# Kernel tuning notes

Measured on AMD Instinct MI355X. Metric: run time of the kernel, lower is better.

Reference implementation:

```python
import jax, jax.numpy as jnp
import numpy as np

B, C, H, W = 16, 256, 64, 64
N = 8                      # num_heads
D = C // N                 # key_dim = head_dim = 32
INIT_VAL, HEADS_RANGE = 1.0, 3.0
SCALING = D ** (-0.5)
EPS = 1e-6


def _rel_pos(h, w):
    # RetNetRelPos2d, chunkwise_recurrent=True branch
    ang = 1.0 / 10000 ** jnp.linspace(0.0, 1.0, D // 2)
    ang = jnp.repeat(ang, 2)                                   # [D]
    idx = jnp.arange(h * w, dtype=jnp.float32)
    sin = jnp.sin(idx[:, None] * ang[None, :]).reshape(h, w, D)
    cos = jnp.cos(idx[:, None] * ang[None, :]).reshape(h, w, D)
    decay = jnp.log(1.0 - 2.0 ** (-INIT_VAL - HEADS_RANGE * jnp.arange(N, dtype=jnp.float32) / N))
    def d1(l):
        i = jnp.arange(l, dtype=jnp.float32)
        return jnp.abs(i[:, None] - i[None, :]) * decay[:, None, None]   # [N,l,l]
    return sin, cos, d1(h), d1(w)


def _rotate_every_two(x):
    x1 = x[..., ::2]
    x2 = x[..., 1::2]
    return jnp.stack([-x2, x1], axis=-1).reshape(x.shape)


def _theta_shift(x, sin, cos):
    return x * cos + _rotate_every_two(x) * sin


def _layernorm(x, g, b):
    m = jnp.mean(x, axis=-1, keepdims=True)
    v = jnp.mean((x - m) ** 2, axis=-1, keepdims=True)
    return g * (x - m) * jax.lax.rsqrt(v + EPS) + b


def setup_inputs() -> dict:
    key = jax.random.key(0)
    ks = jax.random.split(key, 8)
    s = 0.02
    def w(k, shape):
        return (jax.random.normal(k, shape, jnp.float32) * s)
    return {
        "x": jax.random.normal(ks[0], (B, C, H, W), jnp.float32),
        "Wq": w(ks[1], (C, C)), "bq": jnp.zeros((C,), jnp.float32),
        "Wk": w(ks[2], (C, C)), "bk": jnp.zeros((C,), jnp.float32),
        "Wv": w(ks[3], (C, C)), "bv": jnp.zeros((C,), jnp.float32),
        "lepe_w": w(ks[4], (5, 5, 1, C)), "lepe_b": jnp.zeros((C,), jnp.float32),
        "Wo": w(ks[5], (C, C)), "bo": jnp.zeros((C,), jnp.float32),
        "Wfc": w(ks[6], (C, C)), "bfc": jnp.zeros((C,), jnp.float32),
        "g1": jnp.ones((C,), jnp.float32), "b1": jnp.zeros((C,), jnp.float32),
        "g2": jnp.ones((C,), jnp.float32), "b2": jnp.zeros((C,), jnp.float32),
    }


def _vrc(x, sin, cos, mask_h, mask_w, Wq, bq, Wk, bk, Wv, bv, lepe_w, lepe_b, Wo, bo):
    # x: [B,H,W,C]
    b, h, w, _ = x.shape
    q = x @ Wq + bq
    k = (x @ Wk + bk) * SCALING
    v = x @ Wv + bv
    # lepe: depthwise 5x5 conv on v (NHWC)
    lepe = jax.lax.conv_general_dilated(
        v, lepe_w, window_strides=(1, 1), padding=((2, 2), (2, 2)),
        dimension_numbers=("NHWC", "HWIO", "NHWC"), feature_group_count=C) + lepe_b
    # [B,N,H,W,D]
    q = q.reshape(b, h, w, N, D).transpose(0, 3, 1, 2, 4)
    k = k.reshape(b, h, w, N, D).transpose(0, 3, 1, 2, 4)
    qr = _theta_shift(q, sin, cos)
    kr = _theta_shift(k, sin, cos)
    # ---- W-axis attention: [B,H,N,W,W] ----
    qr_w = qr.transpose(0, 2, 1, 3, 4)           # [B,H,N,W,D]
    kr_w = kr.transpose(0, 2, 1, 3, 4)
    v5 = v.reshape(b, h, w, N, D).transpose(0, 1, 3, 2, 4)   # [B,H,N,W,D]
    qk_w = jnp.einsum("bhnqd,bhnkd->bhnqk", qr_w, kr_w) + mask_w
    v5 = jnp.einsum("bhnqk,bhnkd->bhnqd", jax.nn.softmax(qk_w, axis=-1), v5)
    # ---- H-axis attention: [B,W,N,H,H] ----
    qr_h = qr.transpose(0, 3, 1, 2, 4)           # [B,W,N,H,D]
    kr_h = kr.transpose(0, 3, 1, 2, 4)
    v6 = v5.transpose(0, 3, 2, 1, 4)             # [B,W,N,H,D]
    qk_h = jnp.einsum("bwnqd,bwnkd->bwnqk", qr_h, kr_h) + mask_h
    out = jnp.einsum("bwnqk,bwnkd->bwnqd", jax.nn.softmax(qk_h, axis=-1), v6)
    out = out.transpose(0, 3, 1, 2, 4).reshape(b, h, w, C)   # [B,H,W,C]
    return (out + lepe) @ Wo + bo


def reference(x, Wq, bq, Wk, bk, Wv, bv, lepe_w, lepe_b, Wo, bo, Wfc, bfc, g1, b1, g2, b2):
    xt = x.transpose(0, 2, 3, 1)                 # [B,H,W,C]
    sin, cos, mask_h, mask_w = _rel_pos(H, W)
    y = _vrc(xt, sin, cos, mask_h, mask_w, Wq, bq, Wk, bk, Wv, bv, lepe_w, lepe_b, Wo, bo)
    xt = _layernorm(xt + y, g1, b1)
    xt = _layernorm(xt + (xt @ Wfc + bfc), g2, b2)
    return xt.transpose(0, 3, 1, 2)              # [B,C,H,W]
```

## Files before the change

kernel.cpp:

```cpp
#include <hip/hip_runtime.h>
#include <math.h>

#define B_ 16
#define C_ 256
#define N_ 8
#define D_ 32
#define M_ (B_*64*64)
#define SCALING 0.17677669529663687f

typedef short  bf16x8 __attribute__((ext_vector_type(8)));
typedef float  f32x4  __attribute__((ext_vector_type(4)));
typedef unsigned short u16x8 __attribute__((ext_vector_type(8)));

__device__ __forceinline__ unsigned short f2bf(float f) {
    unsigned u = __float_as_uint(f);
    u += 0x7fffu + ((u >> 16) & 1u);
    return (unsigned short)(u >> 16);
}
__device__ __forceinline__ float bf2f(unsigned short h) {
    return __uint_as_float(((unsigned)h) << 16);
}
__device__ __forceinline__ void gld16(const void* g, void* l) {
    __builtin_amdgcn_global_load_lds(
        (const __attribute__((address_space(1))) unsigned*)g,
        (__attribute__((address_space(3))) unsigned*)l, 16, 0, 0);
}

__global__ __launch_bounds__(256) void k_tables(float* __restrict__ sint,
                                                float* __restrict__ cost)
{
    int t = blockIdx.x * 256 + threadIdx.x;
    int p = t >> 5, d = t & 31;
    int j = d >> 1;
    float ang = (float)pow(10000.0, -(double)j / 15.0);
    float arg = (float)p * ang;
    sint[t] = sinf(arg);
    cost[t] = cosf(arg);
}

__global__ __launch_bounds__(256) void k_wcvt(
    const float* __restrict__ Wq, const float* __restrict__ Wk,
    const float* __restrict__ Wv, const float* __restrict__ Wo,
    const float* __restrict__ Wfc,
    unsigned short* __restrict__ Wqt, unsigned short* __restrict__ Wkt,
    unsigned short* __restrict__ Wvt, unsigned short* __restrict__ Wot,
    unsigned short* __restrict__ Wfct)
{
    __shared__ float t[32][33];
    int z = blockIdx.z;
    const float* W = z==0?Wq : z==1?Wk : z==2?Wv : z==3?Wo : Wfc;
    unsigned short* Wt = z==0?Wqt : z==1?Wkt : z==2?Wvt : z==3?Wot : Wfct;
    float sc = (z==1) ? SCALING : 1.0f;
    int tx = threadIdx.x & 31, ty = threadIdx.x >> 5;
    int bx = blockIdx.x * 32;
    int by = blockIdx.y * 32;
    #pragma unroll
    for (int j = 0; j < 4; ++j)
        t[ty + j*8][tx] = W[(by + ty + j*8) * 256 + bx + tx];
    __syncthreads();
    #pragma unroll
    for (int j = 0; j < 4; ++j)
        Wt[(bx + ty + j*8) * 256 + by + tx] = f2bf(t[tx][ty + j*8] * sc);
}

__global__ __launch_bounds__(256) void k_prep(const float* __restrict__ x,
                                              float* __restrict__ xt,
                                              unsigned short* __restrict__ xbf)
{
    __shared__ float t[32][33];
    int tx = threadIdx.x & 31, ty = threadIdx.x >> 5;
    int bx = blockIdx.x * 32;
    int by = blockIdx.y * 32;
    size_t bo = (size_t)blockIdx.z * (256*4096);
    #pragma unroll
    for (int j = 0; j < 4; ++j)
        t[ty + j*8][tx] = x[bo + (size_t)(by + ty + j*8) * 4096 + bx + tx];
    __syncthreads();
    #pragma unroll
    for (int j = 0; j < 4; ++j) {
        float v = t[tx][ty + j*8];
        size_t o = bo + (size_t)(bx + ty + j*8) * 256 + by + tx;
        xt[o] = v;
        xbf[o] = f2bf(v);
    }
}

__device__ __forceinline__ void mfma128(
    const unsigned short* A, const unsigned short* Bt, int r0, int c0,
    unsigned short* As, unsigned short* Bs, f32x4 acc[4][4])
{
    const int tid = threadIdx.x;
    const int w = tid >> 6, l = tid & 63;
    const int wr = w >> 1, wc = w & 1;
    const int fr = l & 15, fq = l >> 4;
    const int lrow  = l >> 3;
    const int lunit = (l & 7) ^ lrow;
    const int sw = fr & 7;
    #pragma unroll
    for (int kt = 0; kt < 256; kt += 64) {
        __syncthreads();
        #pragma unroll
        for (int it = 0; it < 4; ++it) {
            int R0 = 32*w + it*8;
            gld16(A  + (size_t)(r0 + R0 + lrow) * 256 + kt + lunit*8, As + R0*64);
            gld16(Bt + (size_t)(c0 + R0 + lrow) * 256 + kt + lunit*8, Bs + R0*64);
        }
        __syncthreads();
        #pragma unroll
        for (int kk = 0; kk < 2; ++kk) {
            const int u = (kk*4 + fq) ^ sw;
            bf16x8 af[4], bfr[4];
            #pragma unroll
            for (int i = 0; i < 4; ++i)
                af[i] = *(const bf16x8*)(As + (wr*64 + i*16 + fr)*64 + u*8);
            #pragma unroll
            for (int j = 0; j < 4; ++j)
                bfr[j] = *(const bf16x8*)(Bs + (wc*64 + j*16 + fr)*64 + u*8);
            #pragma unroll
            for (int i = 0; i < 4; ++i)
                #pragma unroll
                for (int j = 0; j < 4; ++j)
                    acc[i][j] = __builtin_amdgcn_mfma_f32_16x16x32_bf16(
                        bfr[j], af[i], acc[i][j], 0, 0, 0);
        }
    }
}

__global__ __launch_bounds__(256) void k_qkv(
    const unsigned short* __restrict__ xbf,
    const unsigned short* __restrict__ Wqt, const unsigned short* __restrict__ Wkt,
    const unsigned short* __restrict__ Wvt,
    const float* __restrict__ bq, const float* __restrict__ bk,
    const float* __restrict__ bv,
    unsigned short* __restrict__ qb, unsigned short* __restrict__ kb,
    unsigned short* __restrict__ vb,
    const float* __restrict__ sint, const float* __restrict__ cost)
{
    __shared__ __align__(16) unsigned short As[8192], Bs[8192];
    int z = blockIdx.z;
    const unsigned short* Bt = z==0?Wqt : z==1?Wkt : Wvt;
    const float* bias = z==0?bq : z==1?bk : bv;
    unsigned short* dst = z==0?qb : z==1?kb : vb;
    int r0 = blockIdx.x * 128, c0 = blockIdx.y * 128;

    f32x4 acc[4][4];
    #pragma unroll
    for (int i = 0; i < 4; ++i)
        #pragma unroll
        for (int j = 0; j < 4; ++j) { f32x4 zr = {0.f,0.f,0.f,0.f}; acc[i][j] = zr; }
    mfma128(xbf, Bt, r0, c0, As, Bs, acc);

    int l = threadIdx.x & 63, w = threadIdx.x >> 6;
    int wr = w>>1, wc = w&1, c = l&15, g = l>>4;
    float sc = (z==1) ? SCALING : 1.0f;
    #pragma unroll
    for (int i = 0; i < 4; ++i) {
        int rbase = r0 + wr*64 + i*16 + c;
        int b = rbase >> 12, pos = rbase & 4095;
        #pragma unroll
        for (int j = 0; j < 4; ++j) {
            int nb = c0 + wc*64 + j*16 + g*4;
            int nh = nb >> 5, dl = nb & 31;
            float4 b4 = *(const float4*)(bias + nb);
            f32x4 v = acc[i][j];
            v[0] += b4.x*sc; v[1] += b4.y*sc; v[2] += b4.z*sc; v[3] += b4.w*sc;
            if (z < 2) {
                float4 s4 = *(const float4*)(sint + (size_t)pos*32 + dl);
                float4 c4 = *(const float4*)(cost + (size_t)pos*32 + dl);
                float e0 = v[0]*c4.x - v[1]*s4.x;
                float o0 = v[1]*c4.y + v[0]*s4.y;
                float e1 = v[2]*c4.z - v[3]*s4.z;
                float o1 = v[3]*c4.w + v[2]*s4.w;
                v[0]=e0; v[1]=o0; v[2]=e1; v[3]=o1;
            }
            ushort4 ov = make_ushort4(f2bf(v[0]), f2bf(v[1]), f2bf(v[2]), f2bf(v[3]));
            *(ushort4*)(dst + (size_t)(b*8 + nh)*131072 + (size_t)pos*32 + dl) = ov;
        }
    }
}

__global__ __launch_bounds__(256) void k_gemm_bf(
    const unsigned short* __restrict__ A, const unsigned short* __restrict__ Bt,
    const float* __restrict__ bias, float* __restrict__ out)
{
    __shared__ __align__(16) unsigned short As[8192], Bs[8192];
    int r0 = blockIdx.x * 128, c0 = blockIdx.y * 128;
    f32x4 acc[4][4];
    #pragma unroll
    for (int i = 0; i < 4; ++i)
        #pragma unroll
        for (int j = 0; j < 4; ++j) { f32x4 zr = {0.f,0.f,0.f,0.f}; acc[i][j] = zr; }
    mfma128(A, Bt, r0, c0, As, Bs, acc);
    int l = threadIdx.x & 63, w = threadIdx.x >> 6;
    int wr = w>>1, wc = w&1, c = l&15, g = l>>4;
    #pragma unroll
    for (int i = 0; i < 4; ++i) {
        int m = r0 + wr*64 + i*16 + c;
        #pragma unroll
        for (int j = 0; j < 4; ++j) {
            int nb = c0 + wc*64 + j*16 + g*4;
            float4 b4 = *(const float4*)(bias + nb);
            f32x4 v = acc[i][j];
            float4 o4 = make_float4(v[0]+b4.x, v[1]+b4.y, v[2]+b4.z, v[3]+b4.w);
            *(float4*)(out + (size_t)m*256 + nb) = o4;
        }
    }
}

__global__ __launch_bounds__(256) void k_conv(
    const unsigned short* __restrict__ v, const float* __restrict__ cw,
    const float* __restrict__ cb, float* __restrict__ out)
{
    __shared__ float vs[5*68*36];
    __shared__ float wts[25*32];
    int h = blockIdx.x, n = blockIdx.y, b = blockIdx.z;
    int tid = threadIdx.x;
    for (int i = tid; i < 5*68*36; i += 256) vs[i] = 0.f;
    for (int i = tid; i < 800; i += 256) {
        int tap = i >> 5, d = i & 31;
        wts[i] = cw[tap*256 + n*32 + d];
    }
    __syncthreads();
    const unsigned short* vb_ = v + (size_t)((b*8 + n)*64) * 2048;
    #pragma unroll
    for (int it = 0; it < 5; ++it) {
        int f  = tid + it*256;
        int rr = f >> 8;
        int f2 = f & 255;
        int w  = f2 >> 2, d8 = (f2 & 3) * 8;
        int hh = h + rr - 2;
        if (hh >= 0 && hh < 64) {
            u16x8 vv = *(const u16x8*)(vb_ + hh*2048 + w*32 + d8);
            float* dp = vs + (rr*68 + w + 2)*36 + d8;
            #pragma unroll
            for (int e = 0; e < 8; ++e) dp[e] = bf2f(vv[e]);
        }
    }
    __syncthreads();
    int d = tid & 31, wq = tid >> 5;
    float wreg[25];
    #pragma unroll
    for (int t5 = 0; t5 < 25; ++t5) wreg[t5] = wts[t5*32 + d];
    float bias = cb[n*32 + d];
    for (int w = wq; w < 64; w += 8) {
        float acc = bias;
        #pragma unroll
        for (int dy = 0; dy < 5; ++dy)
            #pragma unroll
            for (int dx = 0; dx < 5; ++dx)
                acc = fmaf(vs[(dy*68 + w + dx)*36 + d], wreg[dy*5+dx], acc);
        out[(size_t)((b*64 + h)*64 + w)*256 + n*32 + d] = acc;
    }
}

__global__ __launch_bounds__(256, 3) void k_attn_mfma(
    const unsigned short* __restrict__ Qb, const unsigned short* __restrict__ Kb,
    const unsigned short* Vb, const float* __restrict__ lepe,
    unsigned short* Ob, int dir)
{
    __shared__ unsigned short S[4 * 4864];
    int tid = threadIdx.x;
    int wv = tid >> 6, l = tid & 63;
    int gid = blockIdx.x * 4 + wv;
    int n = (gid >> 6) & 7;
    int c = l & 15, g = l >> 4;
    size_t base; int sstr;
    if (dir == 0) { base = (size_t)gid * 2048;                               sstr = 32;   }
    else          { base = (size_t)(gid >> 6) * 131072 + (size_t)(gid & 63) * 32; sstr = 2048; }

    unsigned short* Vt = S + wv * 4864;
    unsigned short* Ps = Vt + 2304;

    float decayf = (float)log(1.0 - exp2(-1.0 - 3.0 * (double)n / 8.0));

    #pragma unroll
    for (int it = 0; it < 4; ++it) {
        u16x8 vv = *(const u16x8*)(Vb + base + (size_t)l * sstr + it*8);
        #pragma unroll
        for (int e = 0; e < 8; ++e)
            Vt[(it*8 + e)*72 + l] = vv[e];
    }

    bf16x8 qf[4], kf[4];
    #pragma unroll
    for (int i = 0; i < 4; ++i) {
        qf[i] = *(const bf16x8*)(Qb + base + (size_t)(i*16 + c) * sstr + g*8);
        kf[i] = *(const bf16x8*)(Kb + base + (size_t)(i*16 + c) * sstr + g*8);
    }

    f32x4 acc[4][4];
    #pragma unroll
    for (int i = 0; i < 4; ++i)
        #pragma unroll
        for (int j = 0; j < 4; ++j) { f32x4 zr = {0.f,0.f,0.f,0.f}; acc[i][j] = zr; }
    #pragma unroll
    for (int i = 0; i < 4; ++i)
        #pragma unroll
        for (int j = 0; j < 4; ++j)
            acc[i][j] = __builtin_amdgcn_mfma_f32_16x16x32_bf16(
                qf[i], kf[j], acc[i][j], 0, 0, 0);

    float rinv[4][4];
    #pragma unroll
    for (int i = 0; i < 4; ++i) {
        #pragma unroll
        for (int r = 0; r < 4; ++r) {
            float qi = (float)(i*16 + g*4 + r);
            float m = -1e30f;
            #pragma unroll
            for (int j = 0; j < 4; ++j) {
                float ki = (float)(j*16 + c);
                acc[i][j][r] += fabsf(qi - ki) * decayf;
                m = fmaxf(m, acc[i][j][r]);
            }
            m = fmaxf(m, __shfl_xor(m, 1, 16));
            m = fmaxf(m, __shfl_xor(m, 2, 16));
            m = fmaxf(m, __shfl_xor(m, 4, 16));
            m = fmaxf(m, __shfl_xor(m, 8, 16));
            float s = 0.f;
            #pragma unroll
            for (int j = 0; j < 4; ++j) {
                float e = __expf(acc[i][j][r] - m);
                acc[i][j][r] = e;
                s += e;
            }
            s += __shfl_xor(s, 1, 16);
            s += __shfl_xor(s, 2, 16);
            s += __shfl_xor(s, 4, 16);
            s += __shfl_xor(s, 8, 16);
            rinv[i][r] = 1.f / s;
        }
    }

    f32x4 o[4][2];
    #pragma unroll
    for (int i = 0; i < 4; ++i) { f32x4 zr = {0.f,0.f,0.f,0.f}; o[i][0] = zr; o[i][1] = zr; }
    #pragma unroll
    for (int s = 0; s < 2; ++s) {
        #pragma unroll
        for (int i = 0; i < 4; ++i)
            #pragma unroll
            for (int r = 0; r < 4; ++r)
                #pragma unroll
                for (int jj = 0; jj < 2; ++jj)
                    Ps[(i*16 + g*4 + r)*40 + jj*16 + c] = f2bf(acc[i][2*s + jj][r]);
        bf16x8 vf0 = *(const bf16x8*)(Vt + (     c)*72 + s*32 + g*8);
        bf16x8 vf1 = *(const bf16x8*)(Vt + (16 + c)*72 + s*32 + g*8);
        #pragma unroll
        for (int i = 0; i < 4; ++i) {
            bf16x8 pa = *(const bf16x8*)(Ps + (i*16 + c)*40 + g*8);
            o[i][0] = __builtin_amdgcn_mfma_f32_16x16x32_bf16(pa, vf0, o[i][0], 0, 0, 0);
            o[i][1] = __builtin_amdgcn_mfma_f32_16x16x32_bf16(pa, vf1, o[i][1], 0, 0, 0);
        }
    }

    #pragma unroll
    for (int i = 0; i < 4; ++i) {
        #pragma unroll
        for (int r = 0; r < 4; ++r) {
            int q = i*16 + g*4 + r;
            float ri = rinv[i][r];
            if (dir == 0) {
                Ob[base + (size_t)q*32 + c]      = f2bf(o[i][0][r] * ri);
                Ob[base + (size_t)q*32 + 16 + c] = f2bf(o[i][1][r] * ri);
            } else {
                int b = gid >> 9, w2 = gid & 63;
                size_t idx = ((size_t)((b*64 + q)*64 + w2))*256 + n*32 + c;
                Ob[idx]      = f2bf(o[i][0][r] * ri + lepe[idx]);
                Ob[idx + 16] = f2bf(o[i][1][r] * ri + lepe[idx + 16]);
            }
        }
    }
}

template<bool BFOUT>
__global__ __launch_bounds__(256) void k_ln(
    const float* A, const float* __restrict__ Bv,
    const float* __restrict__ g, const float* __restrict__ bb,
    float* out, unsigned short* __restrict__ outbf)
{
    int row  = blockIdx.x * 4 + (threadIdx.x >> 6);
    int lane = threadIdx.x & 63;
    size_t off = (size_t)row * 256 + lane*4;
    float4 a4 = *(const float4*)(A + off);
    float4 b4 = *(const float4*)(Bv + off);
    float v0=a4.x+b4.x, v1=a4.y+b4.y, v2=a4.z+b4.z, v3=a4.w+b4.w;
    float s = v0+v1+v2+v3;
    #pragma unroll
    for (int mm = 1; mm < 64; mm <<= 1) s += __shfl_xor(s, mm, 64);
    float mean = s * (1.0f/256.0f);
    float d0=v0-mean, d1=v1-mean, d2=v2-mean, d3=v3-mean;
    float qq = d0*d0 + d1*d1 + d2*d2 + d3*d3;
    #pragma unroll
    for (int mm = 1; mm < 64; mm <<= 1) qq += __shfl_xor(qq, mm, 64);
    float rstd = rsqrtf(qq * (1.0f/256.0f) + 1e-6f);
    float4 g4  = *(const float4*)(g + lane*4);
    float4 be4 = *(const float4*)(bb + lane*4);
    float o0 = g4.x*d0*rstd + be4.x, o1 = g4.y*d1*rstd + be4.y;
    float o2 = g4.z*d2*rstd + be4.z, o3 = g4.w*d3*rstd + be4.w;
    *(float4*)(out + off) = make_float4(o0, o1, o2, o3);
    if (BFOUT) {
        ushort4 ov = make_ushort4(f2bf(o0), f2bf(o1), f2bf(o2), f2bf(o3));
        *(ushort4*)(outbf + off) = ov;
    }
}

__global__ __launch_bounds__(256) void k_transpose(const float* __restrict__ src,
                                                   float* __restrict__ dst,
                                                   int rows, int cols)
{
    __shared__ float t[32][33];
    int tx = threadIdx.x & 31, ty = threadIdx.x >> 5;
    int bx = blockIdx.x * 32, by = blockIdx.y * 32;
    size_t bo = (size_t)blockIdx.z * rows * cols;
    #pragma unroll
    for (int j = 0; j < 4; ++j)
        t[ty + j*8][tx] = src[bo + (size_t)(by + ty + j*8) * cols + bx + tx];
    __syncthreads();
    #pragma unroll
    for (int j = 0; j < 4; ++j)
        dst[bo + (size_t)(bx + ty + j*8) * rows + by + tx] = t[tx][ty + j*8];
}

extern "C" void kernel_launch(void* const* d_in, const int* in_sizes, int n_in,
                              void* d_out, int out_size, void* d_ws, size_t ws_size,
                              hipStream_t stream)
{
    (void)in_sizes; (void)n_in; (void)out_size;
    const float* x   = (const float*)d_in[0];
    const float* Wq  = (const float*)d_in[1];
    const float* bq  = (const float*)d_in[2];
    const float* Wk  = (const float*)d_in[3];
    const float* bk  = (const float*)d_in[4];
    const float* Wv  = (const float*)d_in[5];
    const float* bv  = (const float*)d_in[6];
    const float* lw  = (const float*)d_in[7];
    const float* lb  = (const float*)d_in[8];
    const float* Wo  = (const float*)d_in[9];
    const float* bo  = (const float*)d_in[10];
    const float* Wfc = (const float*)d_in[11];
    const float* bfc = (const float*)d_in[12];
    const float* g1  = (const float*)d_in[13];
    const float* b1  = (const float*)d_in[14];
    const float* g2  = (const float*)d_in[15];
    const float* b2  = (const float*)d_in[16];
    float* out = (float*)d_out;

    const size_t NBB = 67108864;
    const size_t NEED = 3*NBB + 2*524288 + 5*131072;
    if (ws_size < NEED) return;

    char* wsb = (char*)d_ws;
    float*          xt   = (float*)wsb;
    unsigned short* xbf  = (unsigned short*)(wsb + NBB);
    unsigned short* qb   = (unsigned short*)(wsb + NBB + NBB/2);
    unsigned short* kb   = (unsigned short*)(wsb + 2*NBB);
    unsigned short* vb   = (unsigned short*)(wsb + 2*NBB + NBB/2);
    float*          yb   = (float*)(wsb + NBB + NBB/2);
    float* sint = (float*)(wsb + 3*NBB);
    float* cost = sint + 131072;
    unsigned short* Wqt  = (unsigned short*)(cost + 131072);
    unsigned short* Wkt  = Wqt + 65536;
    unsigned short* Wvt  = Wkt + 65536;
    unsigned short* Wot  = Wvt + 65536;
    unsigned short* Wfct = Wot + 65536;

    k_tables<<<512, 256, 0, stream>>>(sint, cost);
    k_wcvt<<<dim3(8,8,5), 256, 0, stream>>>(Wq,Wk,Wv,Wo,Wfc,
                                            Wqt,Wkt,Wvt,Wot,Wfct);
    k_prep<<<dim3(128,8,16), 256, 0, stream>>>(x, xt, xbf);
    k_qkv<<<dim3(512,2,3), 256, 0, stream>>>(xbf, Wqt,Wkt,Wvt, bq,bk,bv,
                                             qb,kb,vb, sint,cost);
    k_conv<<<dim3(64,8,16), 256, 0, stream>>>(vb, lw, lb, out);
    k_attn_mfma<<<2048, 256, 0, stream>>>(qb, kb, vb, nullptr, vb, 0);
    k_attn_mfma<<<2048, 256, 0, stream>>>(qb, kb, vb, out, xbf, 1);
    k_gemm_bf<<<dim3(512,2), 256, 0, stream>>>(xbf, Wot, bo, yb);
    k_ln<true><<<16384, 256, 0, stream>>>(xt, yb, g1, b1, xt, xbf);
    k_gemm_bf<<<dim3(512,2), 256, 0, stream>>>(xbf, Wfct, bfc, out);
    k_ln<false><<<16384, 256, 0, stream>>>(xt, out, g2, b2, yb, nullptr);
    k_transpose<<<dim3(8,128,16), 256, 0, stream>>>(yb, out, 4096, 256);
}
```

Baseline: 519.8 us.

## Fuse output and FC GEMMs with residual LayerNorm and final transpose

Replaces the two 128x128-tiled GEMMs plus separate LayerNorm and transpose kernels with a single GEMM kernel per stage. Each block computes a full 128x256 row tile, so the residual add and LayerNorm can be done in the epilogue through a cross-wave reduction in shared memory. The second stage writes straight to the NCHW output layout. This removes several full-tensor fp32 round trips and three launches. In exchange it uses a single-pass variance (E[x^2]-mean^2), strided scalar stores for the transposed output, and in-place reads and writes of xt and xbf within the same kernel. It also raises the attention kernel's occupancy hint.

```diff
diff --git a/kernel.cpp b/kernel.cpp
--- a/kernel.cpp
+++ b/kernel.cpp
@@ -179,30 +179,123 @@
     }
 }
 
-__global__ __launch_bounds__(256) void k_gemm_bf(
-    const unsigned short* __restrict__ A, const unsigned short* __restrict__ Bt,
-    const float* __restrict__ bias, float* __restrict__ out)
-{
-    __shared__ __align__(16) unsigned short As[8192], Bs[8192];
-    int r0 = blockIdx.x * 128, c0 = blockIdx.y * 128;
+template<int TMODE>
+__global__ __launch_bounds__(512, 4) void k_gemm_ln(
+    const unsigned short* Abf,
+    const unsigned short* __restrict__ Bt,
+    const float* __restrict__ bias,
+    const float* resid,
+    const float* __restrict__ gg, const float* __restrict__ be,
+    float* outf, unsigned short* outbf)
+{
+    __shared__ __align__(16) unsigned short As[8192], Bs[16384];
+    __shared__ float red_s[4][128], red_q[4][128];
+    const int tid = threadIdx.x, w = tid >> 6, l = tid & 63;
+    const int wr = w >> 2, wc = w & 3;
+    const int fr = l & 15, fq = l >> 4;
+    const int lrow = l >> 3, lunit = (l & 7) ^ lrow;
+    const int r0 = blockIdx.x * 128;
+
     f32x4 acc[4][4];
     #pragma unroll
     for (int i = 0; i < 4; ++i)
         #pragma unroll
         for (int j = 0; j < 4; ++j) { f32x4 zr = {0.f,0.f,0.f,0.f}; acc[i][j] = zr; }
-    mfma128(A, Bt, r0, c0, As, Bs, acc);
-    int l = threadIdx.x & 63, w = threadIdx.x >> 6;
-    int wr = w>>1, wc = w&1, c = l&15, g = l>>4;
+
+    #pragma unroll
+    for (int kt = 0; kt < 256; kt += 64) {
+        __syncthreads();
+        #pragma unroll
+        for (int it = 0; it < 2; ++it) {
+            int R0 = 8*w + it*64;
+            gld16(Abf + (size_t)(r0 + R0 + lrow) * 256 + kt + lunit*8, As + R0*64);
+        }
+        #pragma unroll
+        for (int it = 0; it < 4; ++it) {
+            int R0 = 8*w + it*64;
+            gld16(Bt + (size_t)(R0 + lrow) * 256 + kt + lunit*8, Bs + R0*64);
+        }
+        __syncthreads();
+        #pragma unroll
+        for (int kk = 0; kk < 2; ++kk) {
+            const int u = (kk*4 + fq) ^ (fr & 7);
+            bf16x8 af[4], bfr[4];
+            #pragma unroll
+            for (int i = 0; i < 4; ++i)
+                af[i] = *(const bf16x8*)(As + (wr*64 + i*16 + fr)*64 + u*8);
+            #pragma unroll
+            for (int j = 0; j < 4; ++j)
+                bfr[j] = *(const bf16x8*)(Bs + (wc*64 + j*16 + fr)*64 + u*8);
+            #pragma unroll
+            for (int i = 0; i < 4; ++i)
+                #pragma unroll
+                for (int j = 0; j < 4; ++j)
+                    acc[i][j] = __builtin_amdgcn_mfma_f32_16x16x32_bf16(
+                        bfr[j], af[i], acc[i][j], 0, 0, 0);
+        }
+    }
+
+    const int c = l & 15, g4 = l >> 4;
+    float psum[4], pq[4];
     #pragma unroll
     for (int i = 0; i < 4; ++i) {
         int m = r0 + wr*64 + i*16 + c;
+        psum[i] = 0.f; pq[i] = 0.f;
         #pragma unroll
         for (int j = 0; j < 4; ++j) {
-            int nb = c0 + wc*64 + j*16 + g*4;
+            int nb = wc*64 + j*16 + g4*4;
             float4 b4 = *(const float4*)(bias + nb);
+            float4 x4 = *(const float4*)(resid + (size_t)m*256 + nb);
             f32x4 v = acc[i][j];
-            float4 o4 = make_float4(v[0]+b4.x, v[1]+b4.y, v[2]+b4.z, v[3]+b4.w);
-            *(float4*)(out + (size_t)m*256 + nb) = o4;
+            v[0] += b4.x + x4.x; v[1] += b4.y + x4.y;
+            v[2] += b4.z + x4.z; v[3] += b4.w + x4.w;
+            acc[i][j] = v;
+            psum[i] += v[0]+v[1]+v[2]+v[3];
+            pq[i]   += v[0]*v[0]+v[1]*v[1]+v[2]*v[2]+v[3]*v[3];
+        }
+        psum[i] += __shfl_xor(psum[i], 16); psum[i] += __shfl_xor(psum[i], 32);
+        pq[i]   += __shfl_xor(pq[i], 16);   pq[i]   += __shfl_xor(pq[i], 32);
+    }
+    if (l < 16) {
+        #pragma unroll
+        for (int i = 0; i < 4; ++i) {
+            red_s[wc][wr*64 + i*16 + l] = psum[i];
+            red_q[wc][wr*64 + i*16 + l] = pq[i];
+        }
+    }
+    __syncthreads();
+
+    #pragma unroll
+    for (int i = 0; i < 4; ++i) {
+        int ml = wr*64 + i*16 + c;
+        int m  = r0 + ml;
+        float S = red_s[0][ml] + red_s[1][ml] + red_s[2][ml] + red_s[3][ml];
+        float Q = red_q[0][ml] + red_q[1][ml] + red_q[2][ml] + red_q[3][ml];
+        float mean = S * (1.f/256.f);
+        float var  = Q * (1.f/256.f) - mean*mean;
+        float rstd = rsqrtf(var + 1e-6f);
+        #pragma unroll
+        for (int j = 0; j < 4; ++j) {
+            int nb = wc*64 + j*16 + g4*4;
+            float4 gv = *(const float4*)(gg + nb);
+            float4 bv = *(const float4*)(be + nb);
+            f32x4 v = acc[i][j];
+            float o0 = gv.x*(v[0]-mean)*rstd + bv.x;
+            float o1 = gv.y*(v[1]-mean)*rstd + bv.y;
+            float o2 = gv.z*(v[2]-mean)*rstd + bv.z;
+            float o3 = gv.w*(v[3]-mean)*rstd + bv.w;
+            if (TMODE == 0) {
+                *(float4*)(outf + (size_t)m*256 + nb) = make_float4(o0,o1,o2,o3);
+                *(ushort4*)(outbf + (size_t)m*256 + nb) =
+                    make_ushort4(f2bf(o0), f2bf(o1), f2bf(o2), f2bf(o3));
+            } else {
+                int b = m >> 12, pos = m & 4095;
+                size_t obase = ((size_t)b*256 + nb) * 4096 + pos;
+                outf[obase]          = o0;
+                outf[obase + 4096]   = o1;
+                outf[obase + 8192]   = o2;
+                outf[obase + 12288]  = o3;
+            }
         }
     }
 }
@@ -253,7 +346,7 @@
     }
 }
 
-__global__ __launch_bounds__(256, 3) void k_attn_mfma(
+__global__ __launch_bounds__(256, 4) void k_attn_mfma(
     const unsigned short* __restrict__ Qb, const unsigned short* __restrict__ Kb,
     const unsigned short* Vb, const float* __restrict__ lepe,
     unsigned short* Ob, int dir)
@@ -371,55 +464,6 @@
             }
         }
     }
-}
-
-template<bool BFOUT>
-__global__ __launch_bounds__(256) void k_ln(
-    const float* A, const float* __restrict__ Bv,
-    const float* __restrict__ g, const float* __restrict__ bb,
-    float* out, unsigned short* __restrict__ outbf)
-{
-    int row  = blockIdx.x * 4 + (threadIdx.x >> 6);
-    int lane = threadIdx.x & 63;
-    size_t off = (size_t)row * 256 + lane*4;
-    float4 a4 = *(const float4*)(A + off);
-    float4 b4 = *(const float4*)(Bv + off);
-    float v0=a4.x+b4.x, v1=a4.y+b4.y, v2=a4.z+b4.z, v3=a4.w+b4.w;
-    float s = v0+v1+v2+v3;
-    #pragma unroll
-    for (int mm = 1; mm < 64; mm <<= 1) s += __shfl_xor(s, mm, 64);
-    float mean = s * (1.0f/256.0f);
-    float d0=v0-mean, d1=v1-mean, d2=v2-mean, d3=v3-mean;
-    float qq = d0*d0 + d1*d1 + d2*d2 + d3*d3;
-    #pragma unroll
-    for (int mm = 1; mm < 64; mm <<= 1) qq += __shfl_xor(qq, mm, 64);
-    float rstd = rsqrtf(qq * (1.0f/256.0f) + 1e-6f);
-    float4 g4  = *(const float4*)(g + lane*4);
-    float4 be4 = *(const float4*)(bb + lane*4);
-    float o0 = g4.x*d0*rstd + be4.x, o1 = g4.y*d1*rstd + be4.y;
-    float o2 = g4.z*d2*rstd + be4.z, o3 = g4.w*d3*rstd + be4.w;
-    *(float4*)(out + off) = make_float4(o0, o1, o2, o3);
-    if (BFOUT) {
-        ushort4 ov = make_ushort4(f2bf(o0), f2bf(o1), f2bf(o2), f2bf(o3));
-        *(ushort4*)(outbf + off) = ov;
-    }
-}
-
-__global__ __launch_bounds__(256) void k_transpose(const float* __restrict__ src,
-                                                   float* __restrict__ dst,
-                                                   int rows, int cols)
-{
-    __shared__ float t[32][33];
-    int tx = threadIdx.x & 31, ty = threadIdx.x >> 5;
-    int bx = blockIdx.x * 32, by = blockIdx.y * 32;
-    size_t bo = (size_t)blockIdx.z * rows * cols;
-    #pragma unroll
-    for (int j = 0; j < 4; ++j)
-        t[ty + j*8][tx] = src[bo + (size_t)(by + ty + j*8) * cols + bx + tx];
-    __syncthreads();
-    #pragma unroll
-    for (int j = 0; j < 4; ++j)
-        dst[bo + (size_t)(bx + ty + j*8) * rows + by + tx] = t[tx][ty + j*8];
 }
 
 extern "C" void kernel_launch(void* const* d_in, const int* in_sizes, int n_in,
@@ -456,7 +500,6 @@
     unsigned short* qb   = (unsigned short*)(wsb + NBB + NBB/2);
     unsigned short* kb   = (unsigned short*)(wsb + 2*NBB);
     unsigned short* vb   = (unsigned short*)(wsb + 2*NBB + NBB/2);
-    float*          yb   = (float*)(wsb + NBB + NBB/2);
     float* sint = (float*)(wsb + 3*NBB);
     float* cost = sint + 131072;
     unsigned short* Wqt  = (unsigned short*)(cost + 131072);
@@ -474,9 +517,6 @@
     k_conv<<<dim3(64,8,16), 256, 0, stream>>>(vb, lw, lb, out);
     k_attn_mfma<<<2048, 256, 0, stream>>>(qb, kb, vb, nullptr, vb, 0);
     k_attn_mfma<<<2048, 256, 0, stream>>>(qb, kb, vb, out, xbf, 1);
-    k_gemm_bf<<<dim3(512,2), 256, 0, stream>>>(xbf, Wot, bo, yb);
-    k_ln<true><<<16384, 256, 0, stream>>>(xt, yb, g1, b1, xt, xbf);
-    k_gemm_bf<<<dim3(512,2), 256, 0, stream>>>(xbf, Wfct, bfc, out);
-    k_ln<false><<<16384, 256, 0, stream>>>(xt, out, g2, b2, yb, nullptr);
-    k_transpose<<<dim3(8,128,16), 256, 0, stream>>>(yb, out, 4096, 256);
-}
+    k_gemm_ln<0><<<512, 512, 0, stream>>>(xbf, Wot, bo, xt, g1, b1, xt, xbf);
+    k_gemm_ln<1><<<512, 512, 0, stream>>>(xbf, Wfct, bfc, xt, g2, b2, out, nullptr);
+}
```

Result: faster. 496.9 us (-4.4%).
